# Kernel optimization log

Hardware: AMD Instinct MI355X
Metric: run time of the kernel (lower is better)

The kernel has to match this reference:

```python
import jax, jax.numpy as jnp
import numpy as np

B, N, D = 1, 4096, 320
HEADS, DIM_HEAD = 8, 40
PHASE, Hm, Wm = 3, 64, 64  # guidance mask spatial dims; Hm*Wm == N


def setup_inputs() -> dict:
    key = jax.random.key(0)
    ks = jax.random.split(key, 7)
    s = 0.02
    x = jax.random.normal(ks[0], (B, N, D), jnp.float32)
    guidance_mask = jax.random.bernoulli(ks[1], 0.25, (B, PHASE, Hm, Wm)).astype(jnp.float32)
    Wq = jax.random.normal(ks[2], (D, HEADS * DIM_HEAD), jnp.float32) * s
    Wk = jax.random.normal(ks[3], (D, HEADS * DIM_HEAD), jnp.float32) * s
    Wv = jax.random.normal(ks[4], (D, HEADS * DIM_HEAD), jnp.float32) * s
    Wo = jax.random.normal(ks[5], (HEADS * DIM_HEAD, D), jnp.float32) * s
    bo = jnp.zeros((D,), jnp.float32)
    return {"x": x, "guidance_mask": guidance_mask, "Wq": Wq, "Wk": Wk,
            "Wv": Wv, "Wo": Wo, "bo": bo}


def reference(x, guidance_mask, Wq, Wk, Wv, Wo, bo):
    b, n, _ = x.shape
    h, dh = HEADS, DIM_HEAD
    scale = dh ** (-0.5)

    def split_heads(t):
        # b n (h d) -> (b h) n d
        return t.reshape(b, n, h, dh).transpose(0, 2, 1, 3).reshape(b * h, n, dh)

    q = split_heads(x @ Wq)
    k = split_heads(x @ Wk)
    v = split_heads(x @ Wv)

    sim = jnp.einsum('bid,bjd->bij', q, k) * scale  # (b*h, n, n)

    _, p, Hh, Ww = guidance_mask.shape
    HW = Hh * Ww  # == n
    g = guidance_mask.reshape(b, p, HW)
    # sum over phases of outer products, clamped at 1 (binary block mask)
    mask_sim = jnp.minimum(jnp.einsum('bpi,bpj->bij', g, g), 1.0)  # (b, HW, HW)
    mask_sim = jnp.repeat(mask_sim, h, axis=0)  # (b*h, HW, HW), heads within each b

    neg = -jnp.finfo(sim.dtype).max
    # original: sim[:, :, :HW][mask_sim == 0] = -max ; here n == HW so full matrix
    sim = jnp.where(mask_sim == 0, neg, sim)

    attn = jax.nn.softmax(sim, axis=-1)
    out = jnp.einsum('bij,bjd->bid', attn, v)  # (b*h, n, dh)
    out = out.reshape(b, h, n, dh).transpose(0, 2, 1, 3).reshape(b, n, h * dh)
    return out @ Wo + bo
```

## Files before the change

### kernel.cpp

```cpp
#include <hip/hip_runtime.h>
#include <hip/hip_bf16.h>
#include <stdint.h>

#define NT 4096
#define DM 320
#define NH 8
#define DH 40
#define KS 4
#define QSCALE 0.22811013f
#define PSTR 68
#define KFJB 640

typedef float f32x4 __attribute__((ext_vector_type(4)));
typedef __bf16 bf16x8 __attribute__((ext_vector_type(8)));

__device__ __forceinline__ unsigned short f2b(float f) {
  unsigned u = __builtin_bit_cast(unsigned, f);
  u += 0x7FFFu + ((u >> 16) & 1u);
  return (unsigned short)(u >> 16);
}

__device__ __forceinline__ bf16x8 ld_bf8(const unsigned short* p) {
  uint4 v = *(const uint4*)p;
  return __builtin_bit_cast(bf16x8, v);
}

__device__ __forceinline__ f32x4 mfma16(bf16x8 a, bf16x8 b, f32x4 c) {
  return __builtin_amdgcn_mfma_f32_16x16x32_bf16(a, b, c, 0, 0, 0);
}

__device__ __forceinline__ float fexp2(float x) {
#if __has_builtin(__builtin_amdgcn_exp2f)
  return __builtin_amdgcn_exp2f(x);
#else
  float r; asm("v_exp_f32 %0, %1" : "=v"(r) : "v"(x)); return r;
#endif
}

__device__ __forceinline__ uint2 pack4(float a, float b, float c, float d) {
  uint2 pk;
  pk.x = (unsigned)f2b(a) | ((unsigned)f2b(b) << 16);
  pk.y = (unsigned)f2b(c) | ((unsigned)f2b(d) << 16);
  return pk;
}

__device__ __forceinline__ size_t fmi(int tile, int nk, int k, int o) {
  return ((size_t)tile * nk + (k >> 5)) * 512 + (size_t)((k >> 3) & 3) * 128 +
         (size_t)(o & 15) * 8 + (k & 7);
}

__global__ __launch_bounds__(256) void prep_kernel(
    const float* __restrict__ x, const float* __restrict__ g,
    const float* __restrict__ Wq, const float* __restrict__ Wk,
    const float* __restrict__ Wv, const float* __restrict__ Wo,
    unsigned short* __restrict__ xbf, unsigned char* __restrict__ sigb,
    unsigned short* __restrict__ Wtf) {
  __shared__ __align__(16) unsigned short lt[64 * 72];
  const int b = blockIdx.x, t = threadIdx.x;
  if (b < 1280) {
    int i = (b * 256 + t) * 4;
    int m = i / DM, k = i % DM;
    float4 v = *(const float4*)(x + i);
    ushort4 u;
    u.x = f2b(v.x); u.y = f2b(v.y); u.z = f2b(v.z); u.w = f2b(v.w);
    *(ushort4*)(xbf + fmi(m >> 4, 10, k, m)) = u;
    return;
  }
  if (b < 1296) {
    int i = (b - 1280) * 256 + t;
    unsigned s = 0;
    if (g[i] != 0.f)          s |= 1u;
    if (g[NT + i] != 0.f)     s |= 2u;
    if (g[2 * NT + i] != 0.f) s |= 4u;
    sigb[i] = (unsigned char)s;
    return;
  }
  int bb = b - 1296;
  int kx = bb % 5, cy = bb / 5;
  int cm = cy % 5;
  const float* src;
  int rowbase;
  if (cy < 5)       { src = Wq; rowbase = cm * 64; }
  else if (cy < 10) { src = Wk; rowbase = 320 + cm * 64; }
  else if (cy < 15) { src = Wv; rowbase = 640 + cm * 64; }
  else              { src = Wo; rowbase = 960 + cm * 64; }
  const int c0 = cm * 64;
  const int k0 = kx * 64;
#pragma unroll
  for (int i = 0; i < 4; ++i) {
    int kr = (t >> 4) + i * 16, cc = (t & 15) * 4;
    float4 w4 = *(const float4*)&src[(size_t)(k0 + kr) * DM + c0 + cc];
    lt[(cc + 0) * 72 + kr] = f2b(w4.x);
    lt[(cc + 1) * 72 + kr] = f2b(w4.y);
    lt[(cc + 2) * 72 + kr] = f2b(w4.z);
    lt[(cc + 3) * 72 + kr] = f2b(w4.w);
  }
  __syncthreads();
#pragma unroll
  for (int i = 0; i < 2; ++i) {
    int idx = t + i * 256, cl = idx >> 3, ch = idx & 7;
    int c = rowbase + cl, k = k0 + ch * 8;
    *(uint4*)&Wtf[fmi(c >> 4, 10, k, c)] = *(const uint4*)&lt[cl * 72 + ch * 8];
  }
}

__global__ __launch_bounds__(256, 4) void qkv_gemm(
    const unsigned short* __restrict__ xbf, const unsigned short* __restrict__ Wtf,
    unsigned short* __restrict__ Qf, unsigned short* __restrict__ Kf,
    unsigned short* __restrict__ Vf) {
  const int t = threadIdx.x;
  const int w = t >> 6, lane = t & 63, quad = lane >> 4, ln = lane & 15;
  const int m0 = blockIdx.x * 64;
  const int cy = blockIdx.y;
  const int a = cy / 5;
  const int cc0 = (cy % 5) * 64;
  const int mt = (m0 >> 4) + w;
  const int ct0 = a * 20 + (cc0 >> 4);

  f32x4 acc[4] = {{0,0,0,0},{0,0,0,0},{0,0,0,0},{0,0,0,0}};
  for (int kc = 0; kc < 10; ++kc) {
    bf16x8 xf = ld_bf8(xbf + ((size_t)(mt * 10 + kc)) * 512 + lane * 8);
#pragma unroll
    for (int nt = 0; nt < 4; ++nt) {
      bf16x8 wf = ld_bf8(Wtf + ((size_t)((ct0 + nt) * 10 + kc)) * 512 + lane * 8);
      if (a < 2) acc[nt] = mfma16(wf, xf, acc[nt]);
      else       acc[nt] = mfma16(xf, wf, acc[nt]);
    }
  }
  if (a == 0) {
    const int m = m0 + w * 16 + ln;
#pragma unroll
    for (int nt = 0; nt < 4; ++nt) {
      int c = cc0 + nt * 16 + quad * 4;
      int h = c / DH, d = c % DH;
      uint2 pk = pack4(acc[nt][0] * QSCALE, acc[nt][1] * QSCALE,
                       acc[nt][2] * QSCALE, acc[nt][3] * QSCALE);
      *(uint2*)&Qf[fmi(h * 256 + (m >> 4), 2, d, m)] = pk;
    }
  } else if (a == 1) {
    const int m = m0 + w * 16 + ln;
#pragma unroll
    for (int nt = 0; nt < 4; ++nt) {
      int c = cc0 + nt * 16 + quad * 4;
      int h = c / DH, d = c % DH;
      uint2 pk = pack4(acc[nt][0], acc[nt][1], acc[nt][2], acc[nt][3]);
      size_t base = ((size_t)h * 256 + (m >> 4)) * KFJB;
      size_t idx = (d < 32)
          ? base + (size_t)(d >> 3) * 128 + (size_t)(m & 15) * 8 + (d & 7)
          : base + 512 + (size_t)(m & 15) * 8 + (d - 32);
      *(uint2*)&Kf[idx] = pk;
    }
  } else {
    const int mb = m0 + w * 16 + quad * 4;
#pragma unroll
    for (int nt = 0; nt < 4; ++nt) {
      int c = cc0 + nt * 16 + ln;
      int h = c / DH, d = c % DH;
      uint2 pk = pack4(acc[nt][0], acc[nt][1], acc[nt][2], acc[nt][3]);
      size_t idx = ((((((size_t)(h * 64 + (mb >> 6)) * 3 + (d >> 4)) * 2 +
                       ((mb >> 5) & 1)) * 4 + ((mb >> 3) & 3)) * 16 + (d & 15))) * 8 +
                   (mb & 7);
      *(uint2*)&Vf[idx] = pk;
    }
  }
}

__global__ __launch_bounds__(256, 4) void attn_kernel(
    const unsigned short* __restrict__ Qf, const unsigned short* __restrict__ Kf,
    const unsigned short* __restrict__ Vf, const unsigned char* __restrict__ sigb,
    unsigned short* __restrict__ Opf, float* __restrict__ Lpart) {
  __shared__ __align__(16) unsigned short pt[4][32 * PSTR];
  const int t = threadIdx.x;
  const int w = t >> 6, lane = t & 63, quad = lane >> 4, ln = lane & 15;
  const int h = blockIdx.y, qt = blockIdx.x, sp = blockIdx.z;
  const int qrow = qt * 128 + w * 32;
  const int j0 = sp * 16;

  const unsigned short* Kfh = Kf + (size_t)h * 256 * KFJB;
  const unsigned short* Vfh = Vf + (size_t)h * 196608;
  unsigned short* ptw = pt[w];
  const uint4 z4 = {0, 0, 0, 0};
  const uint4 ones4 = {0x3F803F80u, 0x3F803F80u, 0x3F803F80u, 0x3F803F80u};
  const bool vone = (ln == 8);

  bf16x8 qa[2][2];
  unsigned sqx4[2], uqx4[2];
  f32x4 o[3][2] = {{{0,0,0,0},{0,0,0,0}},{{0,0,0,0},{0,0,0,0}},{{0,0,0,0},{0,0,0,0}}};

#pragma unroll
  for (int tq = 0; tq < 2; ++tq) {
    int row = qrow + tq * 16 + ln;
    size_t qbase = ((size_t)(h * 256 + qt * 8 + w * 2 + tq) * 2) * 512;
    qa[tq][0] = ld_bf8(Qf + qbase + lane * 8);
    uint4 q1 = z4;
    if (quad == 0) q1 = *(const uint4*)(Qf + qbase + 512 + lane * 8);
    qa[tq][1] = __builtin_bit_cast(bf16x8, q1);
    unsigned s = sigb[row];
    sqx4[tq] = s * 0x01010101u;
    uqx4[tq] = (s == 0u) ? 0xFFFFFFFFu : 0u;
    if (s == 0u) {
      qa[tq][0] = __builtin_bit_cast(bf16x8, z4);
      qa[tq][1] = __builtin_bit_cast(bf16x8, z4);
    }
  }

  for (int jt = j0; jt < j0 + 16; ++jt) {
    uint4 kfr0[4], kfr1[4];
#pragma unroll
    for (int nt = 0; nt < 4; ++nt) {
      const unsigned short* kb = Kfh + (size_t)(jt * 4 + nt) * KFJB;
      kfr0[nt] = *(const uint4*)(kb + lane * 8);
      kfr1[nt] = z4;
      if (lane < 16) kfr1[nt] = *(const uint4*)(kb + 512 + lane * 8);
    }

#pragma unroll
    for (int nt = 0; nt < 4; ++nt) {
      bf16x8 ka0 = __builtin_bit_cast(bf16x8, kfr0[nt]);
      bf16x8 ka1 = __builtin_bit_cast(bf16x8, kfr1[nt]);
      unsigned spj = *(const unsigned*)(sigb + jt * 64 + nt * 16 + quad * 4);
#pragma unroll
      for (int tq = 0; tq < 2; ++tq) {
        f32x4 acc = {0.f, 0.f, 0.f, 0.f};
        acc = mfma16(ka0, qa[tq][0], acc);
        acc = mfma16(ka1, qa[tq][1], acc);
        unsigned m4 = (spj & sqx4[tq]) | uqx4[tq];
        unsigned u[4];
#pragma unroll
        for (int r = 0; r < 4; ++r) {
          unsigned mb = (m4 >> (8 * r)) & 255u;
          float am = mb ? acc[r] : -3.0e38f;
          u[r] = __builtin_bit_cast(unsigned, fexp2(am));
        }
        uint2 pk;
        pk.x = (u[0] >> 16) | (u[1] & 0xffff0000u);
        pk.y = (u[2] >> 16) | (u[3] & 0xffff0000u);
        *(uint2*)&ptw[(tq * 16 + ln) * PSTR + nt * 16 + quad * 4] = pk;
      }
    }
    uint4 vfr[6];
#pragma unroll
    for (int ot = 0; ot < 3; ++ot)
#pragma unroll
      for (int c = 0; c < 2; ++c)
        vfr[ot * 2 + c] =
            *(const uint4*)(Vfh + ((size_t)((jt * 3 + ot) * 2 + c)) * 512 + lane * 8);
    if (vone) { vfr[4] = ones4; vfr[5] = ones4; }

    asm volatile("s_waitcnt lgkmcnt(0)" ::: "memory");
    bf16x8 pb[2][2];
#pragma unroll
    for (int tq = 0; tq < 2; ++tq) {
      pb[tq][0] = ld_bf8(&ptw[(tq * 16 + ln) * PSTR + quad * 8]);
      pb[tq][1] = ld_bf8(&ptw[(tq * 16 + ln) * PSTR + 32 + quad * 8]);
    }
#pragma unroll
    for (int ot = 0; ot < 3; ++ot) {
      bf16x8 va0 = __builtin_bit_cast(bf16x8, vfr[ot * 2]);
      bf16x8 va1 = __builtin_bit_cast(bf16x8, vfr[ot * 2 + 1]);
#pragma unroll
      for (int tq = 0; tq < 2; ++tq) {
        o[ot][tq] = mfma16(va0, pb[tq][0], o[ot][tq]);
        o[ot][tq] = mfma16(va1, pb[tq][1], o[ot][tq]);
      }
    }
  }

#pragma unroll
  for (int tq = 0; tq < 2; ++tq) {
    int m = qrow + tq * 16 + ln;
#pragma unroll
    for (int ot = 0; ot < 3; ++ot) {
      int d0 = ot * 16 + quad * 4;
      if (d0 < DH) {
        int c = h * DH + d0;
        uint2 pk = pack4(o[ot][tq][0], o[ot][tq][1], o[ot][tq][2], o[ot][tq][3]);
        *(uint2*)&Opf[fmi(sp * 256 + (m >> 4), 10, c, m)] = pk;
      }
    }
    if (quad == 2)
      Lpart[sp * NT + m] = o[2][tq][0];
  }
}

__global__ __launch_bounds__(256, 4) void out_gemm(
    const unsigned short* __restrict__ Opf, const float* __restrict__ Lpart,
    const unsigned short* __restrict__ Wtf, const float* __restrict__ bo,
    float* __restrict__ out) {
  const int t = threadIdx.x;
  const int w = t >> 6, lane = t & 63, quad = lane >> 4, ln = lane & 15;
  const int m0 = blockIdx.x * 64;
  const int cc0 = blockIdx.y * 64;
  const int mt = (m0 >> 4) + w;
  const int m = m0 + w * 16 + ln;
  const int ct0 = 60 + (cc0 >> 4);
  float ls = 0.f;
#pragma unroll
  for (int sp = 0; sp < KS; ++sp) ls += Lpart[sp * NT + m];
  const float inv = 1.f / ls;

  f32x4 acc[4] = {{0,0,0,0},{0,0,0,0},{0,0,0,0},{0,0,0,0}};
  for (int kc = 0; kc < 10; ++kc) {
    float s8[8] = {0, 0, 0, 0, 0, 0, 0, 0};
#pragma unroll
    for (int sp = 0; sp < KS; ++sp) {
      uint4 v = *(const uint4*)(Opf + ((size_t)((sp * 256 + mt) * 10 + kc)) * 512 +
                                lane * 8);
      unsigned vv[4] = {v.x, v.y, v.z, v.w};
#pragma unroll
      for (int j = 0; j < 4; ++j) {
        s8[2 * j]     += __builtin_bit_cast(float, vv[j] << 16);
        s8[2 * j + 1] += __builtin_bit_cast(float, vv[j] & 0xffff0000u);
      }
    }
    unsigned short af8[8];
#pragma unroll
    for (int j = 0; j < 8; ++j) af8[j] = f2b(s8[j] * inv);
    bf16x8 af = ld_bf8(af8);
#pragma unroll
    for (int nt = 0; nt < 4; ++nt) {
      bf16x8 wf = ld_bf8(Wtf + ((size_t)((ct0 + nt) * 10 + kc)) * 512 + lane * 8);
      acc[nt] = mfma16(wf, af, acc[nt]);
    }
  }
#pragma unroll
  for (int nt = 0; nt < 4; ++nt) {
    int c = cc0 + nt * 16 + quad * 4;
    float4 bv = *(const float4*)(bo + c);
    float4 ov;
    ov.x = acc[nt][0] + bv.x;
    ov.y = acc[nt][1] + bv.y;
    ov.z = acc[nt][2] + bv.z;
    ov.w = acc[nt][3] + bv.w;
    *(float4*)(out + (size_t)m * DM + c) = ov;
  }
}

extern "C" void kernel_launch(void* const* d_in, const int* in_sizes, int n_in,
                              void* d_out, int out_size, void* d_ws, size_t ws_size,
                              hipStream_t stream) {
  const float* x  = (const float*)d_in[0];
  const float* g  = (const float*)d_in[1];
  const float* Wq = (const float*)d_in[2];
  const float* Wk = (const float*)d_in[3];
  const float* Wv = (const float*)d_in[4];
  const float* Wo = (const float*)d_in[5];
  const float* bo = (const float*)d_in[6];
  float* out = (float*)d_out;

  char* ws = (char*)d_ws;
  const size_t SIG_OFF = 0;
  const size_t XBF_OFF = 16384;
  const size_t WTF_OFF = XBF_OFF + (size_t)NT * DM * 2;
  const size_t QF_OFF  = WTF_OFF + (size_t)1280 * DM * 2;
  const size_t KF_OFF  = QF_OFF + (size_t)NH * 256 * 2 * 512 * 2;
  const size_t VF_OFF  = KF_OFF + (size_t)NH * 256 * KFJB * 2;
  const size_t OPF_OFF = VF_OFF + (size_t)NH * 196608 * 2;
  const size_t LP_OFF  = OPF_OFF + (size_t)KS * 256 * 10 * 512 * 2;
  unsigned char* sigb  = (unsigned char*)(ws + SIG_OFF);
  unsigned short* xbf  = (unsigned short*)(ws + XBF_OFF);
  unsigned short* Wtf  = (unsigned short*)(ws + WTF_OFF);
  unsigned short* Qf   = (unsigned short*)(ws + QF_OFF);
  unsigned short* Kf   = (unsigned short*)(ws + KF_OFF);
  unsigned short* Vf   = (unsigned short*)(ws + VF_OFF);
  unsigned short* Opf  = (unsigned short*)(ws + OPF_OFF);
  float* Lpart         = (float*)(ws + LP_OFF);

  prep_kernel<<<1396, 256, 0, stream>>>(x, g, Wq, Wk, Wv, Wo, xbf, sigb, Wtf);
  qkv_gemm<<<dim3(64, 15), 256, 0, stream>>>(xbf, Wtf, Qf, Kf, Vf);
  attn_kernel<<<dim3(32, NH, KS), 256, 0, stream>>>(Qf, Kf, Vf, sigb, Opf, Lpart);
  out_gemm<<<dim3(64, 5), 256, 0, stream>>>(Opf, Lpart, Wtf, bo, out);
}
```

Before: 144.1 us.

## Fuse prep conversion into QKV and output GEMMs, dropping prep kernel

```diff
diff --git a/kernel.cpp b/kernel.cpp
--- a/kernel.cpp
+++ b/kernel.cpp
@@ -10,6 +10,7 @@
 #define QSCALE 0.22811013f
 #define PSTR 68
 #define KFJB 640
+#define WSTR 330
 
 typedef float f32x4 __attribute__((ext_vector_type(4)));
 typedef __bf16 bf16x8 __attribute__((ext_vector_type(8)));
@@ -49,80 +50,56 @@
          (size_t)(o & 15) * 8 + (k & 7);
 }
 
-__global__ __launch_bounds__(256) void prep_kernel(
+__global__ __launch_bounds__(256, 3) void qkv_gemm(
     const float* __restrict__ x, const float* __restrict__ g,
     const float* __restrict__ Wq, const float* __restrict__ Wk,
-    const float* __restrict__ Wv, const float* __restrict__ Wo,
-    unsigned short* __restrict__ xbf, unsigned char* __restrict__ sigb,
-    unsigned short* __restrict__ Wtf) {
-  __shared__ __align__(16) unsigned short lt[64 * 72];
-  const int b = blockIdx.x, t = threadIdx.x;
-  if (b < 1280) {
-    int i = (b * 256 + t) * 4;
-    int m = i / DM, k = i % DM;
-    float4 v = *(const float4*)(x + i);
-    ushort4 u;
-    u.x = f2b(v.x); u.y = f2b(v.y); u.z = f2b(v.z); u.w = f2b(v.w);
-    *(ushort4*)(xbf + fmi(m >> 4, 10, k, m)) = u;
+    const float* __restrict__ Wv,
+    unsigned char* __restrict__ sigb, unsigned short* __restrict__ Qf,
+    unsigned short* __restrict__ Kf, unsigned short* __restrict__ Vf) {
+  __shared__ __align__(16) unsigned short wt[64 * WSTR];
+  const int t = threadIdx.x;
+  const int cy = blockIdx.y;
+  if (cy == 15) {
+    if (blockIdx.x < 16) {
+      int i = blockIdx.x * 256 + t;
+      unsigned s = 0;
+      if (g[i] != 0.f)          s |= 1u;
+      if (g[NT + i] != 0.f)     s |= 2u;
+      if (g[2 * NT + i] != 0.f) s |= 4u;
+      sigb[i] = (unsigned char)s;
+    }
     return;
   }
-  if (b < 1296) {
-    int i = (b - 1280) * 256 + t;
-    unsigned s = 0;
-    if (g[i] != 0.f)          s |= 1u;
-    if (g[NT + i] != 0.f)     s |= 2u;
-    if (g[2 * NT + i] != 0.f) s |= 4u;
-    sigb[i] = (unsigned char)s;
-    return;
-  }
-  int bb = b - 1296;
-  int kx = bb % 5, cy = bb / 5;
-  int cm = cy % 5;
-  const float* src;
-  int rowbase;
-  if (cy < 5)       { src = Wq; rowbase = cm * 64; }
-  else if (cy < 10) { src = Wk; rowbase = 320 + cm * 64; }
-  else if (cy < 15) { src = Wv; rowbase = 640 + cm * 64; }
-  else              { src = Wo; rowbase = 960 + cm * 64; }
-  const int c0 = cm * 64;
-  const int k0 = kx * 64;
-#pragma unroll
-  for (int i = 0; i < 4; ++i) {
-    int kr = (t >> 4) + i * 16, cc = (t & 15) * 4;
-    float4 w4 = *(const float4*)&src[(size_t)(k0 + kr) * DM + c0 + cc];
-    lt[(cc + 0) * 72 + kr] = f2b(w4.x);
-    lt[(cc + 1) * 72 + kr] = f2b(w4.y);
-    lt[(cc + 2) * 72 + kr] = f2b(w4.z);
-    lt[(cc + 3) * 72 + kr] = f2b(w4.w);
-  }
-  __syncthreads();
-#pragma unroll
-  for (int i = 0; i < 2; ++i) {
-    int idx = t + i * 256, cl = idx >> 3, ch = idx & 7;
-    int c = rowbase + cl, k = k0 + ch * 8;
-    *(uint4*)&Wtf[fmi(c >> 4, 10, k, c)] = *(const uint4*)&lt[cl * 72 + ch * 8];
-  }
-}
-
-__global__ __launch_bounds__(256, 4) void qkv_gemm(
-    const unsigned short* __restrict__ xbf, const unsigned short* __restrict__ Wtf,
-    unsigned short* __restrict__ Qf, unsigned short* __restrict__ Kf,
-    unsigned short* __restrict__ Vf) {
-  const int t = threadIdx.x;
   const int w = t >> 6, lane = t & 63, quad = lane >> 4, ln = lane & 15;
   const int m0 = blockIdx.x * 64;
-  const int cy = blockIdx.y;
   const int a = cy / 5;
   const int cc0 = (cy % 5) * 64;
-  const int mt = (m0 >> 4) + w;
-  const int ct0 = a * 20 + (cc0 >> 4);
-
+  const float* Wsrc = (a == 0) ? Wq : ((a == 1) ? Wk : Wv);
+
+#pragma unroll
+  for (int i = 0; i < 20; ++i) {
+    int k = (t >> 4) + i * 16;
+    int c4 = (t & 15) * 4;
+    float4 w4 = *(const float4*)&Wsrc[(size_t)k * DM + cc0 + c4];
+    wt[(c4 + 0) * WSTR + k] = f2b(w4.x);
+    wt[(c4 + 1) * WSTR + k] = f2b(w4.y);
+    wt[(c4 + 2) * WSTR + k] = f2b(w4.z);
+    wt[(c4 + 3) * WSTR + k] = f2b(w4.w);
+  }
+  __syncthreads();
+
+  const float* Arow = x + (size_t)(m0 + w * 16 + ln) * DM + quad * 8;
   f32x4 acc[4] = {{0,0,0,0},{0,0,0,0},{0,0,0,0},{0,0,0,0}};
   for (int kc = 0; kc < 10; ++kc) {
-    bf16x8 xf = ld_bf8(xbf + ((size_t)(mt * 10 + kc)) * 512 + lane * 8);
-#pragma unroll
-    for (int nt = 0; nt < 4; ++nt) {
-      bf16x8 wf = ld_bf8(Wtf + ((size_t)((ct0 + nt) * 10 + kc)) * 512 + lane * 8);
+    float4 a0 = *(const float4*)(Arow + kc * 32);
+    float4 a1 = *(const float4*)(Arow + kc * 32 + 4);
+    unsigned short af8[8];
+    af8[0] = f2b(a0.x); af8[1] = f2b(a0.y); af8[2] = f2b(a0.z); af8[3] = f2b(a0.w);
+    af8[4] = f2b(a1.x); af8[5] = f2b(a1.y); af8[6] = f2b(a1.z); af8[7] = f2b(a1.w);
+    bf16x8 xf = ld_bf8(af8);
+#pragma unroll
+    for (int nt = 0; nt < 4; ++nt) {
+      bf16x8 wf = ld_bf8(&wt[(nt * 16 + ln) * WSTR + kc * 32 + quad * 8]);
       if (a < 2) acc[nt] = mfma16(wf, xf, acc[nt]);
       else       acc[nt] = mfma16(xf, wf, acc[nt]);
     }
@@ -285,19 +262,31 @@
 
 __global__ __launch_bounds__(256, 4) void out_gemm(
     const unsigned short* __restrict__ Opf, const float* __restrict__ Lpart,
-    const unsigned short* __restrict__ Wtf, const float* __restrict__ bo,
+    const float* __restrict__ Wo, const float* __restrict__ bo,
     float* __restrict__ out) {
+  __shared__ __align__(16) unsigned short wt[64 * WSTR];
   const int t = threadIdx.x;
   const int w = t >> 6, lane = t & 63, quad = lane >> 4, ln = lane & 15;
   const int m0 = blockIdx.x * 64;
   const int cc0 = blockIdx.y * 64;
   const int mt = (m0 >> 4) + w;
   const int m = m0 + w * 16 + ln;
-  const int ct0 = 60 + (cc0 >> 4);
+
+#pragma unroll
+  for (int i = 0; i < 20; ++i) {
+    int k = (t >> 4) + i * 16;
+    int c4 = (t & 15) * 4;
+    float4 w4 = *(const float4*)&Wo[(size_t)k * DM + cc0 + c4];
+    wt[(c4 + 0) * WSTR + k] = f2b(w4.x);
+    wt[(c4 + 1) * WSTR + k] = f2b(w4.y);
+    wt[(c4 + 2) * WSTR + k] = f2b(w4.z);
+    wt[(c4 + 3) * WSTR + k] = f2b(w4.w);
+  }
   float ls = 0.f;
 #pragma unroll
   for (int sp = 0; sp < KS; ++sp) ls += Lpart[sp * NT + m];
   const float inv = 1.f / ls;
+  __syncthreads();
 
   f32x4 acc[4] = {{0,0,0,0},{0,0,0,0},{0,0,0,0},{0,0,0,0}};
   for (int kc = 0; kc < 10; ++kc) {
@@ -319,7 +308,7 @@
     bf16x8 af = ld_bf8(af8);
 #pragma unroll
     for (int nt = 0; nt < 4; ++nt) {
-      bf16x8 wf = ld_bf8(Wtf + ((size_t)((ct0 + nt) * 10 + kc)) * 512 + lane * 8);
+      bf16x8 wf = ld_bf8(&wt[(nt * 16 + ln) * WSTR + kc * 32 + quad * 8]);
       acc[nt] = mfma16(wf, af, acc[nt]);
     }
   }
@@ -350,24 +339,19 @@
 
   char* ws = (char*)d_ws;
   const size_t SIG_OFF = 0;
-  const size_t XBF_OFF = 16384;
-  const size_t WTF_OFF = XBF_OFF + (size_t)NT * DM * 2;
-  const size_t QF_OFF  = WTF_OFF + (size_t)1280 * DM * 2;
+  const size_t QF_OFF  = 16384;
   const size_t KF_OFF  = QF_OFF + (size_t)NH * 256 * 2 * 512 * 2;
   const size_t VF_OFF  = KF_OFF + (size_t)NH * 256 * KFJB * 2;
   const size_t OPF_OFF = VF_OFF + (size_t)NH * 196608 * 2;
   const size_t LP_OFF  = OPF_OFF + (size_t)KS * 256 * 10 * 512 * 2;
   unsigned char* sigb  = (unsigned char*)(ws + SIG_OFF);
-  unsigned short* xbf  = (unsigned short*)(ws + XBF_OFF);
-  unsigned short* Wtf  = (unsigned short*)(ws + WTF_OFF);
   unsigned short* Qf   = (unsigned short*)(ws + QF_OFF);
   unsigned short* Kf   = (unsigned short*)(ws + KF_OFF);
   unsigned short* Vf   = (unsigned short*)(ws + VF_OFF);
   unsigned short* Opf  = (unsigned short*)(ws + OPF_OFF);
   float* Lpart         = (float*)(ws + LP_OFF);
 
-  prep_kernel<<<1396, 256, 0, stream>>>(x, g, Wq, Wk, Wv, Wo, xbf, sigb, Wtf);
-  qkv_gemm<<<dim3(64, 15), 256, 0, stream>>>(xbf, Wtf, Qf, Kf, Vf);
+  qkv_gemm<<<dim3(64, 16), 256, 0, stream>>>(x, g, Wq, Wk, Wv, sigb, Qf, Kf, Vf);
   attn_kernel<<<dim3(32, NH, KS), 256, 0, stream>>>(Qf, Kf, Vf, sigb, Opf, Lpart);
-  out_gemm<<<dim3(64, 5), 256, 0, stream>>>(Opf, Lpart, Wtf, bo, out);
-}
+  out_gemm<<<dim3(64, 5), 256, 0, stream>>>(Opf, Lpart, Wo, bo, out);
+}
```

After: 152.6 us. 5.9% more time.

## Unroll attention key loop by two with double-buffered P tiles; coarsen prep blocks

Applied to the files above, without the earlier changes.

```diff
diff --git a/kernel.cpp b/kernel.cpp
--- a/kernel.cpp
+++ b/kernel.cpp
@@ -57,17 +57,21 @@
     unsigned short* __restrict__ Wtf) {
   __shared__ __align__(16) unsigned short lt[64 * 72];
   const int b = blockIdx.x, t = threadIdx.x;
-  if (b < 1280) {
-    int i = (b * 256 + t) * 4;
-    int m = i / DM, k = i % DM;
-    float4 v = *(const float4*)(x + i);
-    ushort4 u;
-    u.x = f2b(v.x); u.y = f2b(v.y); u.z = f2b(v.z); u.w = f2b(v.w);
-    *(ushort4*)(xbf + fmi(m >> 4, 10, k, m)) = u;
+  if (b >= 116) {
+    int base = (b - 116) * 2560;
+#pragma unroll
+    for (int j = 0; j < 10; ++j) {
+      int i = (base + j * 256 + t) * 4;
+      int m = i / DM, k = i % DM;
+      float4 v = *(const float4*)(x + i);
+      ushort4 u;
+      u.x = f2b(v.x); u.y = f2b(v.y); u.z = f2b(v.z); u.w = f2b(v.w);
+      *(ushort4*)(xbf + fmi(m >> 4, 10, k, m)) = u;
+    }
     return;
   }
-  if (b < 1296) {
-    int i = (b - 1280) * 256 + t;
+  if (b >= 100) {
+    int i = (b - 100) * 256 + t;
     unsigned s = 0;
     if (g[i] != 0.f)          s |= 1u;
     if (g[NT + i] != 0.f)     s |= 2u;
@@ -75,8 +79,7 @@
     sigb[i] = (unsigned char)s;
     return;
   }
-  int bb = b - 1296;
-  int kx = bb % 5, cy = bb / 5;
+  int kx = b % 5, cy = b / 5;
   int cm = cy % 5;
   const float* src;
   int rowbase;
@@ -169,7 +172,7 @@
     const unsigned short* __restrict__ Qf, const unsigned short* __restrict__ Kf,
     const unsigned short* __restrict__ Vf, const unsigned char* __restrict__ sigb,
     unsigned short* __restrict__ Opf, float* __restrict__ Lpart) {
-  __shared__ __align__(16) unsigned short pt[4][32 * PSTR];
+  __shared__ __align__(16) unsigned short pt[4][2][32 * PSTR];
   const int t = threadIdx.x;
   const int w = t >> 6, lane = t & 63, quad = lane >> 4, ln = lane & 15;
   const int h = blockIdx.y, qt = blockIdx.x, sp = blockIdx.z;
@@ -178,7 +181,6 @@
 
   const unsigned short* Kfh = Kf + (size_t)h * 256 * KFJB;
   const unsigned short* Vfh = Vf + (size_t)h * 196608;
-  unsigned short* ptw = pt[w];
   const uint4 z4 = {0, 0, 0, 0};
   const uint4 ones4 = {0x3F803F80u, 0x3F803F80u, 0x3F803F80u, 0x3F803F80u};
   const bool vone = (ln == 8);
@@ -204,64 +206,72 @@
     }
   }
 
-  for (int jt = j0; jt < j0 + 16; ++jt) {
-    uint4 kfr0[4], kfr1[4];
-#pragma unroll
-    for (int nt = 0; nt < 4; ++nt) {
-      const unsigned short* kb = Kfh + (size_t)(jt * 4 + nt) * KFJB;
-      kfr0[nt] = *(const uint4*)(kb + lane * 8);
-      kfr1[nt] = z4;
-      if (lane < 16) kfr1[nt] = *(const uint4*)(kb + 512 + lane * 8);
-    }
-
-#pragma unroll
-    for (int nt = 0; nt < 4; ++nt) {
-      bf16x8 ka0 = __builtin_bit_cast(bf16x8, kfr0[nt]);
-      bf16x8 ka1 = __builtin_bit_cast(bf16x8, kfr1[nt]);
-      unsigned spj = *(const unsigned*)(sigb + jt * 64 + nt * 16 + quad * 4);
+  for (int jtp = j0; jtp < j0 + 16; jtp += 2) {
+    uint4 vfr[2][6];
+#pragma unroll
+    for (int u = 0; u < 2; ++u) {
+      const int jt = jtp + u;
+      uint4 kfr0[4], kfr1[4];
+#pragma unroll
+      for (int nt = 0; nt < 4; ++nt) {
+        const unsigned short* kb = Kfh + (size_t)(jt * 4 + nt) * KFJB;
+        kfr0[nt] = *(const uint4*)(kb + lane * 8);
+        kfr1[nt] = z4;
+        if (lane < 16) kfr1[nt] = *(const uint4*)(kb + 512 + lane * 8);
+      }
+#pragma unroll
+      for (int ot = 0; ot < 3; ++ot)
+#pragma unroll
+        for (int c = 0; c < 2; ++c)
+          vfr[u][ot * 2 + c] = *(const uint4*)(Vfh +
+              ((size_t)((jt * 3 + ot) * 2 + c)) * 512 + lane * 8);
+      if (vone) { vfr[u][4] = ones4; vfr[u][5] = ones4; }
+
+      unsigned short* ptu = &pt[w][u][0];
+#pragma unroll
+      for (int nt = 0; nt < 4; ++nt) {
+        bf16x8 ka0 = __builtin_bit_cast(bf16x8, kfr0[nt]);
+        bf16x8 ka1 = __builtin_bit_cast(bf16x8, kfr1[nt]);
+        unsigned spj = *(const unsigned*)(sigb + jt * 64 + nt * 16 + quad * 4);
+#pragma unroll
+        for (int tq = 0; tq < 2; ++tq) {
+          f32x4 acc = {0.f, 0.f, 0.f, 0.f};
+          acc = mfma16(ka0, qa[tq][0], acc);
+          acc = mfma16(ka1, qa[tq][1], acc);
+          unsigned m4 = (spj & sqx4[tq]) | uqx4[tq];
+          unsigned uu[4];
+#pragma unroll
+          for (int r = 0; r < 4; ++r) {
+            unsigned mb = (m4 >> (8 * r)) & 255u;
+            float am = mb ? acc[r] : -3.0e38f;
+            uu[r] = __builtin_bit_cast(unsigned, fexp2(am));
+          }
+          uint2 pk;
+          pk.x = (uu[0] >> 16) | (uu[1] & 0xffff0000u);
+          pk.y = (uu[2] >> 16) | (uu[3] & 0xffff0000u);
+          *(uint2*)&ptu[(tq * 16 + ln) * PSTR + nt * 16 + quad * 4] = pk;
+        }
+      }
+    }
+    asm volatile("s_waitcnt lgkmcnt(0)" ::: "memory");
+#pragma unroll
+    for (int u = 0; u < 2; ++u) {
+      unsigned short* ptu = &pt[w][u][0];
+      bf16x8 pb[2][2];
 #pragma unroll
       for (int tq = 0; tq < 2; ++tq) {
-        f32x4 acc = {0.f, 0.f, 0.f, 0.f};
-        acc = mfma16(ka0, qa[tq][0], acc);
-        acc = mfma16(ka1, qa[tq][1], acc);
-        unsigned m4 = (spj & sqx4[tq]) | uqx4[tq];
-        unsigned u[4];
-#pragma unroll
-        for (int r = 0; r < 4; ++r) {
-          unsigned mb = (m4 >> (8 * r)) & 255u;
-          float am = mb ? acc[r] : -3.0e38f;
-          u[r] = __builtin_bit_cast(unsigned, fexp2(am));
+        pb[tq][0] = ld_bf8(&ptu[(tq * 16 + ln) * PSTR + quad * 8]);
+        pb[tq][1] = ld_bf8(&ptu[(tq * 16 + ln) * PSTR + 32 + quad * 8]);
+      }
+#pragma unroll
+      for (int ot = 0; ot < 3; ++ot) {
+        bf16x8 va0 = __builtin_bit_cast(bf16x8, vfr[u][ot * 2]);
+        bf16x8 va1 = __builtin_bit_cast(bf16x8, vfr[u][ot * 2 + 1]);
+#pragma unroll
+        for (int tq = 0; tq < 2; ++tq) {
+          o[ot][tq] = mfma16(va0, pb[tq][0], o[ot][tq]);
+          o[ot][tq] = mfma16(va1, pb[tq][1], o[ot][tq]);
         }
-        uint2 pk;
-        pk.x = (u[0] >> 16) | (u[1] & 0xffff0000u);
-        pk.y = (u[2] >> 16) | (u[3] & 0xffff0000u);
-        *(uint2*)&ptw[(tq * 16 + ln) * PSTR + nt * 16 + quad * 4] = pk;
-      }
-    }
-    uint4 vfr[6];
-#pragma unroll
-    for (int ot = 0; ot < 3; ++ot)
-#pragma unroll
-      for (int c = 0; c < 2; ++c)
-        vfr[ot * 2 + c] =
-            *(const uint4*)(Vfh + ((size_t)((jt * 3 + ot) * 2 + c)) * 512 + lane * 8);
-    if (vone) { vfr[4] = ones4; vfr[5] = ones4; }
-
-    asm volatile("s_waitcnt lgkmcnt(0)" ::: "memory");
-    bf16x8 pb[2][2];
-#pragma unroll
-    for (int tq = 0; tq < 2; ++tq) {
-      pb[tq][0] = ld_bf8(&ptw[(tq * 16 + ln) * PSTR + quad * 8]);
-      pb[tq][1] = ld_bf8(&ptw[(tq * 16 + ln) * PSTR + 32 + quad * 8]);
-    }
-#pragma unroll
-    for (int ot = 0; ot < 3; ++ot) {
-      bf16x8 va0 = __builtin_bit_cast(bf16x8, vfr[ot * 2]);
-      bf16x8 va1 = __builtin_bit_cast(bf16x8, vfr[ot * 2 + 1]);
-#pragma unroll
-      for (int tq = 0; tq < 2; ++tq) {
-        o[ot][tq] = mfma16(va0, pb[tq][0], o[ot][tq]);
-        o[ot][tq] = mfma16(va1, pb[tq][1], o[ot][tq]);
       }
     }
   }
@@ -366,7 +376,7 @@
   unsigned short* Opf  = (unsigned short*)(ws + OPF_OFF);
   float* Lpart         = (float*)(ws + LP_OFF);
 
-  prep_kernel<<<1396, 256, 0, stream>>>(x, g, Wq, Wk, Wv, Wo, xbf, sigb, Wtf);
+  prep_kernel<<<244, 256, 0, stream>>>(x, g, Wq, Wk, Wv, Wo, xbf, sigb, Wtf);
   qkv_gemm<<<dim3(64, 15), 256, 0, stream>>>(xbf, Wtf, Qf, Kf, Vf);
   attn_kernel<<<dim3(32, NH, KS), 256, 0, stream>>>(Qf, Kf, Vf, sigb, Opf, Lpart);
   out_gemm<<<dim3(64, 5), 256, 0, stream>>>(Opf, Lpart, Wtf, bo, out);
```

Result: no change. 146.8 us (+1.9%).

## Permute query rows by mask activity and skip QK/softmax for fully-masked queries

Applied to the files above, without the earlier changes.

```diff
diff --git a/kernel.cpp b/kernel.cpp
--- a/kernel.cpp
+++ b/kernel.cpp
@@ -54,29 +54,59 @@
     const float* __restrict__ Wq, const float* __restrict__ Wk,
     const float* __restrict__ Wv, const float* __restrict__ Wo,
     unsigned short* __restrict__ xbf, unsigned char* __restrict__ sigb,
-    unsigned short* __restrict__ Wtf) {
+    unsigned short* __restrict__ Wtf, int* __restrict__ perm,
+    int* __restrict__ nqp) {
+  const int b = blockIdx.x, t = threadIdx.x;
+  if (b == 100) {
+    __shared__ int cnt[256];
+    unsigned char mys[16];
+    int c1 = 0;
+#pragma unroll
+    for (int i = 0; i < 16; ++i) {
+      int tok = t * 16 + i;
+      unsigned s = 0;
+      if (g[tok] != 0.f)          s |= 1u;
+      if (g[NT + tok] != 0.f)     s |= 2u;
+      if (g[2 * NT + tok] != 0.f) s |= 4u;
+      sigb[tok] = (unsigned char)s;
+      mys[i] = (unsigned char)s;
+      c1 += (s != 0u);
+    }
+    cnt[t] = c1;
+    __syncthreads();
+    for (int off = 1; off < 256; off <<= 1) {
+      int v = (t >= off) ? cnt[t - off] : 0;
+      __syncthreads();
+      cnt[t] += v;
+      __syncthreads();
+    }
+    const int nq = cnt[255];
+    int p1 = cnt[t] - c1;
+    int p0 = nq + (t * 16 - p1);
+#pragma unroll
+    for (int i = 0; i < 16; ++i) {
+      int tok = t * 16 + i;
+      if (mys[i] != 0) perm[p1++] = tok;
+      else             perm[p0++] = tok;
+    }
+    if (t == 0) nqp[0] = nq;
+    return;
+  }
+  if (b > 100) {
+    int base = (b - 101) * 2560;
+#pragma unroll
+    for (int j = 0; j < 10; ++j) {
+      int i = (base + j * 256 + t) * 4;
+      int m = i / DM, k = i % DM;
+      float4 v = *(const float4*)(x + i);
+      ushort4 u;
+      u.x = f2b(v.x); u.y = f2b(v.y); u.z = f2b(v.z); u.w = f2b(v.w);
+      *(ushort4*)(xbf + fmi(m >> 4, 10, k, m)) = u;
+    }
+    return;
+  }
   __shared__ __align__(16) unsigned short lt[64 * 72];
-  const int b = blockIdx.x, t = threadIdx.x;
-  if (b < 1280) {
-    int i = (b * 256 + t) * 4;
-    int m = i / DM, k = i % DM;
-    float4 v = *(const float4*)(x + i);
-    ushort4 u;
-    u.x = f2b(v.x); u.y = f2b(v.y); u.z = f2b(v.z); u.w = f2b(v.w);
-    *(ushort4*)(xbf + fmi(m >> 4, 10, k, m)) = u;
-    return;
-  }
-  if (b < 1296) {
-    int i = (b - 1280) * 256 + t;
-    unsigned s = 0;
-    if (g[i] != 0.f)          s |= 1u;
-    if (g[NT + i] != 0.f)     s |= 2u;
-    if (g[2 * NT + i] != 0.f) s |= 4u;
-    sigb[i] = (unsigned char)s;
-    return;
-  }
-  int bb = b - 1296;
-  int kx = bb % 5, cy = bb / 5;
+  int kx = b % 5, cy = b / 5;
   int cm = cy % 5;
   const float* src;
   int rowbase;
@@ -106,7 +136,7 @@
 
 __global__ __launch_bounds__(256, 4) void qkv_gemm(
     const unsigned short* __restrict__ xbf, const unsigned short* __restrict__ Wtf,
-    unsigned short* __restrict__ Qf, unsigned short* __restrict__ Kf,
+    unsigned short* __restrict__ Qb, unsigned short* __restrict__ Kf,
     unsigned short* __restrict__ Vf) {
   const int t = threadIdx.x;
   const int w = t >> 6, lane = t & 63, quad = lane >> 4, ln = lane & 15;
@@ -135,7 +165,7 @@
       int h = c / DH, d = c % DH;
       uint2 pk = pack4(acc[nt][0] * QSCALE, acc[nt][1] * QSCALE,
                        acc[nt][2] * QSCALE, acc[nt][3] * QSCALE);
-      *(uint2*)&Qf[fmi(h * 256 + (m >> 4), 2, d, m)] = pk;
+      *(uint2*)&Qb[((size_t)h * NT + m) * 64 + d] = pk;
     }
   } else if (a == 1) {
     const int m = m0 + w * 16 + ln;
@@ -166,8 +196,9 @@
 }
 
 __global__ __launch_bounds__(256, 4) void attn_kernel(
-    const unsigned short* __restrict__ Qf, const unsigned short* __restrict__ Kf,
+    const unsigned short* __restrict__ Qb, const unsigned short* __restrict__ Kf,
     const unsigned short* __restrict__ Vf, const unsigned char* __restrict__ sigb,
+    const int* __restrict__ perm, const int* __restrict__ nqp,
     unsigned short* __restrict__ Opf, float* __restrict__ Lpart) {
   __shared__ __align__(16) unsigned short pt[4][32 * PSTR];
   const int t = threadIdx.x;
@@ -175,67 +206,76 @@
   const int h = blockIdx.y, qt = blockIdx.x, sp = blockIdx.z;
   const int qrow = qt * 128 + w * 32;
   const int j0 = sp * 16;
+  const int nq_pad = (nqp[0] + 127) & ~127;
+  const bool writer = (qt * 128 >= nq_pad);
 
   const unsigned short* Kfh = Kf + (size_t)h * 256 * KFJB;
   const unsigned short* Vfh = Vf + (size_t)h * 196608;
   unsigned short* ptw = pt[w];
   const uint4 z4 = {0, 0, 0, 0};
   const uint4 ones4 = {0x3F803F80u, 0x3F803F80u, 0x3F803F80u, 0x3F803F80u};
+  const bf16x8 onesb = __builtin_bit_cast(bf16x8, ones4);
   const bool vone = (ln == 8);
 
   bf16x8 qa[2][2];
   unsigned sqx4[2], uqx4[2];
+  int morig[2];
   f32x4 o[3][2] = {{{0,0,0,0},{0,0,0,0}},{{0,0,0,0},{0,0,0,0}},{{0,0,0,0},{0,0,0,0}}};
 
 #pragma unroll
   for (int tq = 0; tq < 2; ++tq) {
-    int row = qrow + tq * 16 + ln;
-    size_t qbase = ((size_t)(h * 256 + qt * 8 + w * 2 + tq) * 2) * 512;
-    qa[tq][0] = ld_bf8(Qf + qbase + lane * 8);
-    uint4 q1 = z4;
-    if (quad == 0) q1 = *(const uint4*)(Qf + qbase + 512 + lane * 8);
-    qa[tq][1] = __builtin_bit_cast(bf16x8, q1);
-    unsigned s = sigb[row];
-    sqx4[tq] = s * 0x01010101u;
-    uqx4[tq] = (s == 0u) ? 0xFFFFFFFFu : 0u;
-    if (s == 0u) {
-      qa[tq][0] = __builtin_bit_cast(bf16x8, z4);
-      qa[tq][1] = __builtin_bit_cast(bf16x8, z4);
+    int bp = qrow + tq * 16 + ln;
+    int mo = perm[bp];
+    morig[tq] = mo;
+    if (!writer) {
+      const unsigned short* Qp = Qb + ((size_t)h * NT + mo) * 64;
+      qa[tq][0] = ld_bf8(Qp + quad * 8);
+      uint4 q1 = z4;
+      if (quad == 0) q1 = *(const uint4*)(Qp + 32);
+      qa[tq][1] = __builtin_bit_cast(bf16x8, q1);
+      unsigned s = sigb[mo];
+      sqx4[tq] = s * 0x01010101u;
+      uqx4[tq] = (s == 0u) ? 0xFFFFFFFFu : 0u;
+      if (s == 0u) {
+        qa[tq][0] = __builtin_bit_cast(bf16x8, z4);
+        qa[tq][1] = __builtin_bit_cast(bf16x8, z4);
+      }
     }
   }
 
   for (int jt = j0; jt < j0 + 16; ++jt) {
-    uint4 kfr0[4], kfr1[4];
-#pragma unroll
-    for (int nt = 0; nt < 4; ++nt) {
-      const unsigned short* kb = Kfh + (size_t)(jt * 4 + nt) * KFJB;
-      kfr0[nt] = *(const uint4*)(kb + lane * 8);
-      kfr1[nt] = z4;
-      if (lane < 16) kfr1[nt] = *(const uint4*)(kb + 512 + lane * 8);
-    }
-
-#pragma unroll
-    for (int nt = 0; nt < 4; ++nt) {
-      bf16x8 ka0 = __builtin_bit_cast(bf16x8, kfr0[nt]);
-      bf16x8 ka1 = __builtin_bit_cast(bf16x8, kfr1[nt]);
-      unsigned spj = *(const unsigned*)(sigb + jt * 64 + nt * 16 + quad * 4);
-#pragma unroll
-      for (int tq = 0; tq < 2; ++tq) {
-        f32x4 acc = {0.f, 0.f, 0.f, 0.f};
-        acc = mfma16(ka0, qa[tq][0], acc);
-        acc = mfma16(ka1, qa[tq][1], acc);
-        unsigned m4 = (spj & sqx4[tq]) | uqx4[tq];
-        unsigned u[4];
-#pragma unroll
-        for (int r = 0; r < 4; ++r) {
-          unsigned mb = (m4 >> (8 * r)) & 255u;
-          float am = mb ? acc[r] : -3.0e38f;
-          u[r] = __builtin_bit_cast(unsigned, fexp2(am));
+    if (!writer) {
+      uint4 kfr0[4], kfr1[4];
+#pragma unroll
+      for (int nt = 0; nt < 4; ++nt) {
+        const unsigned short* kb = Kfh + (size_t)(jt * 4 + nt) * KFJB;
+        kfr0[nt] = *(const uint4*)(kb + lane * 8);
+        kfr1[nt] = z4;
+        if (lane < 16) kfr1[nt] = *(const uint4*)(kb + 512 + lane * 8);
+      }
+#pragma unroll
+      for (int nt = 0; nt < 4; ++nt) {
+        bf16x8 ka0 = __builtin_bit_cast(bf16x8, kfr0[nt]);
+        bf16x8 ka1 = __builtin_bit_cast(bf16x8, kfr1[nt]);
+        unsigned spj = *(const unsigned*)(sigb + jt * 64 + nt * 16 + quad * 4);
+#pragma unroll
+        for (int tq = 0; tq < 2; ++tq) {
+          f32x4 acc = {0.f, 0.f, 0.f, 0.f};
+          acc = mfma16(ka0, qa[tq][0], acc);
+          acc = mfma16(ka1, qa[tq][1], acc);
+          unsigned m4 = (spj & sqx4[tq]) | uqx4[tq];
+          unsigned u[4];
+#pragma unroll
+          for (int r = 0; r < 4; ++r) {
+            unsigned mb = (m4 >> (8 * r)) & 255u;
+            float am = mb ? acc[r] : -3.0e38f;
+            u[r] = __builtin_bit_cast(unsigned, fexp2(am));
+          }
+          uint2 pk;
+          pk.x = (u[0] >> 16) | (u[1] & 0xffff0000u);
+          pk.y = (u[2] >> 16) | (u[3] & 0xffff0000u);
+          *(uint2*)&ptw[(tq * 16 + ln) * PSTR + nt * 16 + quad * 4] = pk;
         }
-        uint2 pk;
-        pk.x = (u[0] >> 16) | (u[1] & 0xffff0000u);
-        pk.y = (u[2] >> 16) | (u[3] & 0xffff0000u);
-        *(uint2*)&ptw[(tq * 16 + ln) * PSTR + nt * 16 + quad * 4] = pk;
       }
     }
     uint4 vfr[6];
@@ -247,12 +287,16 @@
             *(const uint4*)(Vfh + ((size_t)((jt * 3 + ot) * 2 + c)) * 512 + lane * 8);
     if (vone) { vfr[4] = ones4; vfr[5] = ones4; }
 
-    asm volatile("s_waitcnt lgkmcnt(0)" ::: "memory");
     bf16x8 pb[2][2];
-#pragma unroll
-    for (int tq = 0; tq < 2; ++tq) {
-      pb[tq][0] = ld_bf8(&ptw[(tq * 16 + ln) * PSTR + quad * 8]);
-      pb[tq][1] = ld_bf8(&ptw[(tq * 16 + ln) * PSTR + 32 + quad * 8]);
+    if (!writer) {
+      asm volatile("s_waitcnt lgkmcnt(0)" ::: "memory");
+#pragma unroll
+      for (int tq = 0; tq < 2; ++tq) {
+        pb[tq][0] = ld_bf8(&ptw[(tq * 16 + ln) * PSTR + quad * 8]);
+        pb[tq][1] = ld_bf8(&ptw[(tq * 16 + ln) * PSTR + 32 + quad * 8]);
+      }
+    } else {
+      pb[0][0] = onesb; pb[0][1] = onesb; pb[1][0] = onesb; pb[1][1] = onesb;
     }
 #pragma unroll
     for (int ot = 0; ot < 3; ++ot) {
@@ -268,7 +312,7 @@
 
 #pragma unroll
   for (int tq = 0; tq < 2; ++tq) {
-    int m = qrow + tq * 16 + ln;
+    int m = morig[tq];
 #pragma unroll
     for (int ot = 0; ot < 3; ++ot) {
       int d0 = ot * 16 + quad * 4;
@@ -349,25 +393,31 @@
   float* out = (float*)d_out;
 
   char* ws = (char*)d_ws;
-  const size_t SIG_OFF = 0;
-  const size_t XBF_OFF = 16384;
+  const size_t SIG_OFF  = 0;
+  const size_t NQ_OFF   = 4096;
+  const size_t PERM_OFF = 8192;
+  const size_t XBF_OFF  = 32768;
   const size_t WTF_OFF = XBF_OFF + (size_t)NT * DM * 2;
-  const size_t QF_OFF  = WTF_OFF + (size_t)1280 * DM * 2;
-  const size_t KF_OFF  = QF_OFF + (size_t)NH * 256 * 2 * 512 * 2;
+  const size_t QB_OFF  = WTF_OFF + (size_t)1280 * DM * 2;
+  const size_t KF_OFF  = QB_OFF + (size_t)NH * NT * 64 * 2;
   const size_t VF_OFF  = KF_OFF + (size_t)NH * 256 * KFJB * 2;
   const size_t OPF_OFF = VF_OFF + (size_t)NH * 196608 * 2;
   const size_t LP_OFF  = OPF_OFF + (size_t)KS * 256 * 10 * 512 * 2;
   unsigned char* sigb  = (unsigned char*)(ws + SIG_OFF);
+  int* nqp             = (int*)(ws + NQ_OFF);
+  int* perm            = (int*)(ws + PERM_OFF);
   unsigned short* xbf  = (unsigned short*)(ws + XBF_OFF);
   unsigned short* Wtf  = (unsigned short*)(ws + WTF_OFF);
-  unsigned short* Qf   = (unsigned short*)(ws + QF_OFF);
+  unsigned short* Qb   = (unsigned short*)(ws + QB_OFF);
   unsigned short* Kf   = (unsigned short*)(ws + KF_OFF);
   unsigned short* Vf   = (unsigned short*)(ws + VF_OFF);
   unsigned short* Opf  = (unsigned short*)(ws + OPF_OFF);
   float* Lpart         = (float*)(ws + LP_OFF);
 
-  prep_kernel<<<1396, 256, 0, stream>>>(x, g, Wq, Wk, Wv, Wo, xbf, sigb, Wtf);
-  qkv_gemm<<<dim3(64, 15), 256, 0, stream>>>(xbf, Wtf, Qf, Kf, Vf);
-  attn_kernel<<<dim3(32, NH, KS), 256, 0, stream>>>(Qf, Kf, Vf, sigb, Opf, Lpart);
+  prep_kernel<<<229, 256, 0, stream>>>(x, g, Wq, Wk, Wv, Wo, xbf, sigb, Wtf,
+                                       perm, nqp);
+  qkv_gemm<<<dim3(64, 15), 256, 0, stream>>>(xbf, Wtf, Qb, Kf, Vf);
+  attn_kernel<<<dim3(32, NH, KS), 256, 0, stream>>>(Qb, Kf, Vf, sigb, perm, nqp,
+                                                    Opf, Lpart);
   out_gemm<<<dim3(64, 5), 256, 0, stream>>>(Opf, Lpart, Wtf, bo, out);
 }
```

Result: slower. 147.3 us (+2.2%).
